# Kernel optimization log

Hardware: AMD Instinct MI355X
Metric: run time of the kernel (lower is better)

## Reference

```python
import jax, jax.numpy as jnp
import numpy as np

N, IN, D, H, L, G, FF, E = 50000, 100, 128, 8, 3, 64, 512, 800000


def setup_inputs() -> dict:
    key = jax.random.key(0)
    ks = jax.random.split(key, 12)
    s = 0.02
    x = jax.random.normal(ks[0], (N, IN), dtype=jnp.float32)
    edge_index = jax.random.randint(ks[1], (2, E), 0, N)
    batch = jnp.sort(jax.random.randint(ks[2], (N,), 0, G))
    emb_W = jax.random.normal(ks[3], (IN, D), dtype=jnp.float32) * s
    Wqk = jax.random.normal(ks[4], (L, D, 2 * D), dtype=jnp.float32) * s
    Wv = jax.random.normal(ks[5], (L, D, D), dtype=jnp.float32) * s
    Wo = jax.random.normal(ks[6], (L, D, D), dtype=jnp.float32) * s
    bo = jnp.zeros((L, D), dtype=jnp.float32)
    W1 = jax.random.normal(ks[7], (L, D, FF), dtype=jnp.float32) * s
    b1 = jnp.zeros((L, FF), dtype=jnp.float32)
    W2 = jax.random.normal(ks[8], (L, FF, D), dtype=jnp.float32) * s
    b2 = jnp.zeros((L, D), dtype=jnp.float32)
    return {"x": x, "emb_W": emb_W, "Wqk": Wqk, "Wv": Wv, "Wo": Wo, "bo": bo,
            "W1": W1, "b1": b1, "W2": W2, "b2": b2,
            "edge_index": edge_index, "batch": batch}


def reference(x, emb_W, Wqk, Wv, Wo, bo, W1, b1, W2, b2, edge_index, batch):
    n = x.shape[0]
    d = emb_W.shape[1]
    n_layers = Wqk.shape[0]
    n_heads = H
    hd = d // n_heads
    scale = hd ** (-0.5)
    src, dst = edge_index[0], edge_index[1]  # PyG: j=source, i=target

    h = x @ emb_W  # [n, d]  (dropout is identity in eval)
    for l in range(n_layers):
        qk = h @ Wqk[l]  # [n, 2d]; chunk0 -> _j (source), chunk1 -> _i (target)
        q = qk[:, :d].reshape(n, n_heads, hd)
        k = qk[:, d:].reshape(n, n_heads, hd)
        v = (h @ Wv[l]).reshape(n, n_heads, hd)
        # per-edge attention scores [E, H]
        scores = jnp.sum(k[dst] * q[src], axis=-1) * scale
        # segment softmax over edges sharing a destination node
        m = jax.ops.segment_max(scores, dst, num_segments=n)
        ex = jnp.exp(scores - m[dst])
        denom = jax.ops.segment_sum(ex, dst, num_segments=n)
        attn = ex / (denom[dst] + 1e-16)  # utils.softmax adds 1e-16
        msg = v[src] * attn[:, :, None]  # [E, H, hd]
        out = jax.ops.segment_sum(msg, dst, num_segments=n).reshape(n, d)
        out = out @ Wo[l] + bo[l]
        h = h + out  # norm1 = Identity (batch_norm=True)
        ff = jax.nn.relu(h @ W1[l] + b1[l]) @ W2[l] + b2[l]
        h = h + ff  # norm2 = Identity
    # global mean pool per graph
    n_graphs = G
    sums = jax.ops.segment_sum(h, batch, num_segments=n_graphs)
    cnt = jax.ops.segment_sum(jnp.ones((n, 1), h.dtype), batch, num_segments=n_graphs)
    return sums / jnp.maximum(cnt, 1.0)
```

## Files before the change

kernel.cpp:

```cpp
#include <hip/hip_runtime.h>
#include <math.h>

#define NN 50000
#define NPAD 50048
#define IN_DIM 100
#define DD 128
#define HH 8
#define LL 3
#define GG 64
#define FFD 512
#define EE 800000

typedef __attribute__((ext_vector_type(8))) short bf8_t;
typedef __attribute__((ext_vector_type(4))) float f4_t;

static __device__ __forceinline__ unsigned short f2bf(float f) {
    unsigned u = __builtin_bit_cast(unsigned, f);
    unsigned r = (u + 0x7FFFu + ((u >> 16) & 1u)) >> 16;
    return (unsigned short)r;
}
static __device__ __forceinline__ float bf2f(unsigned short b) {
    unsigned u = ((unsigned)b) << 16;
    return __builtin_bit_cast(float, u);
}

#define GLD16(gsrc, ldst) __builtin_amdgcn_global_load_lds( \
    (const __attribute__((address_space(1))) unsigned int*)(gsrc), \
    (__attribute__((address_space(3))) unsigned int*)(ldst), 16, 0, 0)

__global__ __launch_bounds__(256) void mfma_gemm(
    const unsigned short* __restrict__ Ac,
    const unsigned short* __restrict__ Bc,
    const float* __restrict__ bias,
    const float* __restrict__ resid,
    float* __restrict__ Cf,
    unsigned short* __restrict__ Chl,
    unsigned short* __restrict__ Cb,
    int n, int nk, int M, int do_relu)
{
    __shared__ unsigned short ldsA[128 * 64];
    __shared__ unsigned short ldsB[128 * 64];
    const int tid = threadIdx.x;
    const int lane = tid & 63;
    const int wid = tid >> 6;
    const int wr = (wid >> 1) * 64;
    const int wc = (wid & 1) * 64;
    const long brow = (long)blockIdx.x * 128;
    const long bcol = (long)blockIdx.y * 128;

    f4_t acc[4][4] = {};

    const int srow = tid >> 3;
    const int kbg = (((tid & 7) << 4) ^ ((srow & 7) << 4)) >> 1;
    const int fr = lane & 15;
    const int kq = (lane >> 4) << 4;

    for (int kc = 0; kc < nk; ++kc) {
#pragma unroll
        for (int i = 0; i < 4; ++i) {
            int row = i * 32 + srow;
            GLD16(Ac + ((brow + row) * (size_t)nk + kc) * 64 + kbg,
                  &ldsA[((size_t)i * 256 + tid) * 8]);
            GLD16(Bc + ((bcol + row) * (size_t)nk + kc) * 64 + kbg,
                  &ldsB[((size_t)i * 256 + tid) * 8]);
        }
        __syncthreads();

        bf8_t ah[4], al[4], bh[4], bl[4];
#pragma unroll
        for (int m = 0; m < 4; ++m) {
            int row = wr + m * 16 + fr;
            int sw = (row & 7) << 4;
            ah[m] = *(const bf8_t*)&ldsA[row * 64 + ((kq ^ sw) >> 1)];
            al[m] = *(const bf8_t*)&ldsA[row * 64 + (((kq + 64) ^ sw) >> 1)];
        }
#pragma unroll
        for (int nn = 0; nn < 4; ++nn) {
            int row = wc + nn * 16 + fr;
            int sw = (row & 7) << 4;
            bh[nn] = *(const bf8_t*)&ldsB[row * 64 + ((kq ^ sw) >> 1)];
            bl[nn] = *(const bf8_t*)&ldsB[row * 64 + (((kq + 64) ^ sw) >> 1)];
        }
#pragma unroll
        for (int m = 0; m < 4; ++m)
#pragma unroll
            for (int nn = 0; nn < 4; ++nn) {
                acc[m][nn] = __builtin_amdgcn_mfma_f32_16x16x32_bf16(ah[m], bh[nn], acc[m][nn], 0, 0, 0);
                acc[m][nn] = __builtin_amdgcn_mfma_f32_16x16x32_bf16(al[m], bh[nn], acc[m][nn], 0, 0, 0);
                acc[m][nn] = __builtin_amdgcn_mfma_f32_16x16x32_bf16(ah[m], bl[nn], acc[m][nn], 0, 0, 0);
            }
        __syncthreads();
    }

    const int efr = lane & 15, efq = lane >> 4;
#pragma unroll
    for (int m = 0; m < 4; ++m) {
#pragma unroll
        for (int i = 0; i < 4; ++i) {
            long row = brow + wr + m * 16 + efq * 4 + i;
            if (row >= n) continue;
#pragma unroll
            for (int nn = 0; nn < 4; ++nn) {
                int col = (int)bcol + wc + nn * 16 + efr;
                float v = acc[m][nn][i];
                if (bias) v += bias[col];
                if (do_relu) v = fmaxf(v, 0.f);
                if (resid) v += resid[row * M + col];
                if (Cf) Cf[row * M + col] = v;
                if (Cb) Cb[row * M + col] = f2bf(v);
                if (Chl) {
                    unsigned short hb = f2bf(v);
                    float lo = v - bf2f(hb);
                    size_t cb = (row * (size_t)(M >> 5) + (col >> 5)) * 64 + (col & 31);
                    Chl[cb] = hb;
                    Chl[cb + 32] = f2bf(lo);
                }
            }
        }
    }
}

#define FF_STAGE(T, BUF) do {                                                   \
    _Pragma("unroll")                                                           \
    for (int i_ = 0; i_ < 4; ++i_) {                                            \
        int row_ = i_ * 32 + srow;                                              \
        const unsigned short* srcp_;                                            \
        if ((T) < 4) {                                                          \
            srcp_ = WoT + ((size_t)row_ * 4 + (T)) * 64 + kbg;                  \
        } else {                                                                \
            const int tt_ = (T) - 4;                                            \
            const int c_ = tt_ >> 3, ph_ = (tt_ >> 2) & 1, j_ = tt_ & 3;        \
            srcp_ = (ph_ == 0)                                                  \
                ? W1T + (((size_t)c_ * 128 + row_) * 4 + j_) * 64 + kbg         \
                : W2T + ((size_t)row_ * 16 + (c_ * 4 + j_)) * 64 + kbg;         \
        }                                                                       \
        GLD16(srcp_, &ldsB[BUF][((size_t)i_ * 256 + tid) * 8]);                 \
    }                                                                           \
} while (0)

__global__ __launch_bounds__(256, 2) void ffwo_fused(
    const unsigned short* __restrict__ acp,
    const unsigned short* __restrict__ WoT,
    const unsigned short* __restrict__ W1T,
    const unsigned short* __restrict__ W2T,
    const float* __restrict__ bo,
    const float* __restrict__ b1,
    const float* __restrict__ b2,
    float* __restrict__ h,
    unsigned short* __restrict__ hcout,
    int n)
{
    __shared__ unsigned short ldsB[2][128 * 64];
    __shared__ unsigned short midb[64 * 128];
    __shared__ unsigned short Ahi[64 * 128];

    const int tid = threadIdx.x;
    const int lane = tid & 63;
    const int wid = tid >> 6;
    const int wr = (wid >> 1) * 32;
    const int wc = (wid & 1) * 64;
    const long brow = (long)blockIdx.x * 64;

    const int srow = tid >> 3;
    const int kbg = (((tid & 7) << 4) ^ ((srow & 7) << 4)) >> 1;
    const int fr = lane & 15;
    const int kq = (lane >> 4) << 4;
    const int kq4 = lane >> 4;
    const int efr = lane & 15, efq = lane >> 4;

    bf8_t ahw[2][4];
#pragma unroll
    for (int m = 0; m < 2; ++m) {
        long arow = brow + wr + m * 16 + fr;
#pragma unroll
        for (int kc = 0; kc < 4; ++kc)
            ahw[m][kc] = *(const bf8_t*)&acp[arow * 128 + kc * 32 + kq4 * 8];
    }

    FF_STAGE(0, 0);

    f4_t accW[2][4];
    f4_t acc1[2][4];
    f4_t acc2[2][4];
    f4_t hnew[2][4];
#pragma unroll
    for (int m = 0; m < 2; ++m)
#pragma unroll
        for (int nn = 0; nn < 4; ++nn) {
            accW[m][nn][0] = 0.f; accW[m][nn][1] = 0.f;
            accW[m][nn][2] = 0.f; accW[m][nn][3] = 0.f;
            acc2[m][nn][0] = 0.f; acc2[m][nn][1] = 0.f;
            acc2[m][nn][2] = 0.f; acc2[m][nn][3] = 0.f;
        }

    __syncthreads();

#pragma unroll
    for (int t = 0; t < 36; ++t) {
        const int cur = t & 1;
        if (t < 35) FF_STAGE(t + 1, cur ^ 1);

        if (t < 4) {
            bf8_t bh[4], bl[4];
#pragma unroll
            for (int nn = 0; nn < 4; ++nn) {
                int rowb = wc + nn * 16 + fr;
                int sw = (rowb & 7) << 4;
                bh[nn] = *(const bf8_t*)&ldsB[cur][rowb * 64 + ((kq ^ sw) >> 1)];
                bl[nn] = *(const bf8_t*)&ldsB[cur][rowb * 64 + (((kq + 64) ^ sw) >> 1)];
            }
#pragma unroll
            for (int m = 0; m < 2; ++m)
#pragma unroll
                for (int nn = 0; nn < 4; ++nn) {
                    accW[m][nn] = __builtin_amdgcn_mfma_f32_16x16x32_bf16(ahw[m][t], bh[nn], accW[m][nn], 0, 0, 0);
                    accW[m][nn] = __builtin_amdgcn_mfma_f32_16x16x32_bf16(ahw[m][t], bl[nn], accW[m][nn], 0, 0, 0);
                }
            if (t == 3) {
#pragma unroll
                for (int m = 0; m < 2; ++m)
#pragma unroll
                    for (int i = 0; i < 4; ++i) {
                        int lrow = wr + m * 16 + efq * 4 + i;
                        long row = brow + lrow;
#pragma unroll
                        for (int nn = 0; nn < 4; ++nn) {
                            int col = wc + nn * 16 + efr;
                            float v = accW[m][nn][i] + bo[col] + h[row * 128 + col];
                            hnew[m][nn][i] = v;
                            Ahi[(lrow << 7) + ((((col << 1) ^ ((lrow & 7) << 4))) >> 1)] = f2bf(v);
                        }
                    }
            }
        } else {
            const int tt = t - 4, c = tt >> 3, ph = (tt >> 2) & 1, j = tt & 3;
            if (ph == 0) {
                if (j == 0) {
#pragma unroll
                    for (int m = 0; m < 2; ++m)
#pragma unroll
                        for (int nn = 0; nn < 4; ++nn) {
                            acc1[m][nn][0] = 0.f; acc1[m][nn][1] = 0.f;
                            acc1[m][nn][2] = 0.f; acc1[m][nn][3] = 0.f;
                        }
                }
                bf8_t ah[2], bh[4], bl[4];
#pragma unroll
                for (int m = 0; m < 2; ++m) {
                    int lrow = wr + m * 16 + fr;
                    int kbyte = (j * 64 + kq) ^ ((lrow & 7) << 4);
                    ah[m] = *(const bf8_t*)&Ahi[(lrow << 7) + (kbyte >> 1)];
                }
#pragma unroll
                for (int nn = 0; nn < 4; ++nn) {
                    int rowb = wc + nn * 16 + fr;
                    int sw = (rowb & 7) << 4;
                    bh[nn] = *(const bf8_t*)&ldsB[cur][rowb * 64 + ((kq ^ sw) >> 1)];
                    bl[nn] = *(const bf8_t*)&ldsB[cur][rowb * 64 + (((kq + 64) ^ sw) >> 1)];
                }
#pragma unroll
                for (int m = 0; m < 2; ++m)
#pragma unroll
                    for (int nn = 0; nn < 4; ++nn) {
                        acc1[m][nn] = __builtin_amdgcn_mfma_f32_16x16x32_bf16(ah[m], bh[nn], acc1[m][nn], 0, 0, 0);
                        acc1[m][nn] = __builtin_amdgcn_mfma_f32_16x16x32_bf16(ah[m], bl[nn], acc1[m][nn], 0, 0, 0);
                    }
                if (j == 3) {
#pragma unroll
                    for (int m = 0; m < 2; ++m)
#pragma unroll
                        for (int i = 0; i < 4; ++i) {
                            int lrow = wr + m * 16 + efq * 4 + i;
#pragma unroll
                            for (int nn = 0; nn < 4; ++nn) {
                                int col = wc + nn * 16 + efr;
                                float v = fmaxf(acc1[m][nn][i] + b1[c * 128 + col], 0.f);
                                int e2 = (lrow << 7) + ((((col << 1) ^ ((lrow & 7) << 4))) >> 1);
                                midb[e2] = f2bf(v);
                            }
                        }
                }
            } else {
                bf8_t am[2], bh2[4], bl2[4];
#pragma unroll
                for (int m = 0; m < 2; ++m) {
                    int lrow = wr + m * 16 + fr;
                    int kbyte = (j * 64 + kq) ^ ((lrow & 7) << 4);
                    am[m] = *(const bf8_t*)&midb[(lrow << 7) + (kbyte >> 1)];
                }
#pragma unroll
                for (int nn = 0; nn < 4; ++nn) {
                    int rowb = wc + nn * 16 + fr;
                    int sw = (rowb & 7) << 4;
                    bh2[nn] = *(const bf8_t*)&ldsB[cur][rowb * 64 + ((kq ^ sw) >> 1)];
                    bl2[nn] = *(const bf8_t*)&ldsB[cur][rowb * 64 + (((kq + 64) ^ sw) >> 1)];
                }
#pragma unroll
                for (int m = 0; m < 2; ++m)
#pragma unroll
                    for (int nn = 0; nn < 4; ++nn) {
                        acc2[m][nn] = __builtin_amdgcn_mfma_f32_16x16x32_bf16(am[m], bh2[nn], acc2[m][nn], 0, 0, 0);
                        acc2[m][nn] = __builtin_amdgcn_mfma_f32_16x16x32_bf16(am[m], bl2[nn], acc2[m][nn], 0, 0, 0);
                    }
            }
        }
        __syncthreads();
    }

#pragma unroll
    for (int m = 0; m < 2; ++m)
#pragma unroll
        for (int i = 0; i < 4; ++i) {
            long row = brow + wr + m * 16 + efq * 4 + i;
            if (row >= n) continue;
#pragma unroll
            for (int nn = 0; nn < 4; ++nn) {
                int col = wc + nn * 16 + efr;
                float v = hnew[m][nn][i] + acc2[m][nn][i] + b2[col];
                h[row * 128 + col] = v;
                if (hcout) {
                    unsigned short hb = f2bf(v);
                    size_t cb = (row * (size_t)4 + (col >> 5)) * 64 + (col & 31);
                    hcout[cb] = hb;
                    hcout[cb + 32] = f2bf(v - bf2f(hb));
                }
            }
        }
}

__global__ void cvt_x_kernel(const float* __restrict__ x, unsigned short* __restrict__ xc)
{
    int idx = blockIdx.x * 256 + threadIdx.x;
    if (idx >= NN * 128) return;
    int node = idx >> 7, col = idx & 127;
    float v = (col < IN_DIM) ? x[(size_t)node * IN_DIM + col] : 0.f;
    unsigned short hb = f2bf(v);
    float lo = v - bf2f(hb);
    size_t b = (size_t)node * 256 + (col >> 5) * 64 + (col & 31);
    xc[b] = hb;
    xc[b + 32] = f2bf(lo);
}

struct WDesc { const float* W; unsigned short* Wt; int K, nkpad, M, base; };
struct WDescs { WDesc d[16]; int n; int total; };

__global__ void wcvt_all_kernel(WDescs ds)
{
    int idx = blockIdx.x * 256 + threadIdx.x;
    if (idx >= ds.total) return;
    int di = 0;
    while (di + 1 < ds.n && idx >= ds.d[di + 1].base) ++di;
    WDesc w = ds.d[di];
    int loc = idx - w.base;
    int m = loc % w.M;
    int kc = loc / w.M;
    size_t ob = ((size_t)m * w.nkpad + kc) * 64;
    for (int i = 0; i < 32; ++i) {
        int k = kc * 32 + i;
        float v = (k < w.K) ? w.W[(size_t)k * w.M + m] : 0.f;
        unsigned short hb = f2bf(v);
        w.Wt[ob + i] = hb;
        w.Wt[ob + 32 + i] = f2bf(v - bf2f(hb));
    }
}

__global__ void count_kernel(const int* __restrict__ dst, int* __restrict__ counts)
{
    int e = blockIdx.x * 256 + threadIdx.x;
    if (e < EE) atomicAdd(&counts[dst[e]], 1);
}

__global__ __launch_bounds__(1024) void scan1_kernel(
    const int* __restrict__ counts, int* __restrict__ offsets, int* __restrict__ bsums)
{
    __shared__ int buf[1024];
    int tid = threadIdx.x;
    int i = blockIdx.x * 1024 + tid;
    int v = (i < NN) ? counts[i] : 0;
    buf[tid] = v;
    __syncthreads();
    for (int off = 1; off < 1024; off <<= 1) {
        int t = (tid >= off) ? buf[tid - off] : 0;
        __syncthreads();
        buf[tid] += t;
        __syncthreads();
    }
    if (i < NN) offsets[i + 1] = buf[tid];
    if (tid == 1023) bsums[blockIdx.x] = buf[1023];
}

__global__ void scan2_kernel(int* __restrict__ bsums, int nb)
{
    __shared__ int buf[64];
    int tid = threadIdx.x;
    int v = (tid < nb) ? bsums[tid] : 0;
    buf[tid] = v;
    __syncthreads();
    for (int off = 1; off < 64; off <<= 1) {
        int t = (tid >= off) ? buf[tid - off] : 0;
        __syncthreads();
        buf[tid] += t;
        __syncthreads();
    }
    if (tid < nb) bsums[tid] = buf[tid] - v;
}

__global__ __launch_bounds__(1024) void scan3_kernel(
    int* __restrict__ offsets, const int* __restrict__ bsums)
{
    int i = blockIdx.x * 1024 + threadIdx.x;
    if (i < NN) offsets[i + 1] += bsums[blockIdx.x];
    if (i == 0) offsets[0] = 0;
}

__global__ void fill_kernel(const int* __restrict__ src, const int* __restrict__ dst,
                            const int* __restrict__ offsets, int* __restrict__ cursor,
                            int* __restrict__ csr_src)
{
    int e = blockIdx.x * 256 + threadIdx.x;
    if (e < EE) {
        int d = dst[e];
        int pos = atomicAdd(&cursor[d], 1);
        csr_src[offsets[d] + pos] = src[e];
    }
}

__global__ __launch_bounds__(256) void attn_kernel(
    const unsigned short* __restrict__ QKV,
    const int* __restrict__ offsets, const int* __restrict__ csr_src,
    unsigned short* __restrict__ ac)
{
    int wave = threadIdx.x >> 6;
    int lane = threadIdx.x & 63;
    int node = blockIdx.x * 4 + wave;
    if (node >= NN) return;
    int qoff = ((lane >> 3) << 4) + ((lane & 7) << 1);
    ushort2 k2 = *(const ushort2*)&QKV[(size_t)node * 384 + 128 + qoff];
    float kx = bf2f(k2.x), ky = bf2f(k2.y);
    float m = -INFINITY, s = 0.f, a0 = 0.f, a1 = 0.f;
    int e = offsets[node], end = offsets[node + 1];
    for (; e + 3 < end; e += 4) {
        int j0 = csr_src[e], j1 = csr_src[e + 1], j2 = csr_src[e + 2], j3 = csr_src[e + 3];
        ushort2 q0 = *(const ushort2*)&QKV[(size_t)j0 * 384 + qoff];
        ushort2 q1 = *(const ushort2*)&QKV[(size_t)j1 * 384 + qoff];
        ushort2 q2 = *(const ushort2*)&QKV[(size_t)j2 * 384 + qoff];
        ushort2 q3 = *(const ushort2*)&QKV[(size_t)j3 * 384 + qoff];
        ushort2 v0 = *(const ushort2*)&QKV[(size_t)j0 * 384 + 256 + qoff];
        ushort2 v1 = *(const ushort2*)&QKV[(size_t)j1 * 384 + 256 + qoff];
        ushort2 v2 = *(const ushort2*)&QKV[(size_t)j2 * 384 + 256 + qoff];
        ushort2 v3 = *(const ushort2*)&QKV[(size_t)j3 * 384 + 256 + qoff];
        float p0 = kx * bf2f(q0.x) + ky * bf2f(q0.y);
        float p1 = kx * bf2f(q1.x) + ky * bf2f(q1.y);
        float p2 = kx * bf2f(q2.x) + ky * bf2f(q2.y);
        float p3 = kx * bf2f(q3.x) + ky * bf2f(q3.y);
        p0 += __shfl_xor(p0, 1, 64); p0 += __shfl_xor(p0, 2, 64); p0 += __shfl_xor(p0, 4, 64);
        p1 += __shfl_xor(p1, 1, 64); p1 += __shfl_xor(p1, 2, 64); p1 += __shfl_xor(p1, 4, 64);
        p2 += __shfl_xor(p2, 1, 64); p2 += __shfl_xor(p2, 2, 64); p2 += __shfl_xor(p2, 4, 64);
        p3 += __shfl_xor(p3, 1, 64); p3 += __shfl_xor(p3, 2, 64); p3 += __shfl_xor(p3, 4, 64);
        float sc0 = p0 * 0.25f, sc1 = p1 * 0.25f, sc2 = p2 * 0.25f, sc3 = p3 * 0.25f;
        float mx = fmaxf(fmaxf(fmaxf(sc0, sc1), fmaxf(sc2, sc3)), m);
        float corr = __expf(m - mx);
        float w0 = __expf(sc0 - mx), w1 = __expf(sc1 - mx);
        float w2 = __expf(sc2 - mx), w3 = __expf(sc3 - mx);
        s  = s  * corr + (w0 + w1) + (w2 + w3);
        a0 = a0 * corr + w0 * bf2f(v0.x) + w1 * bf2f(v1.x) + w2 * bf2f(v2.x) + w3 * bf2f(v3.x);
        a1 = a1 * corr + w0 * bf2f(v0.y) + w1 * bf2f(v1.y) + w2 * bf2f(v2.y) + w3 * bf2f(v3.y);
        m = mx;
    }
    if (e + 1 < end) {
        int j0 = csr_src[e], j1 = csr_src[e + 1];
        ushort2 q0 = *(const ushort2*)&QKV[(size_t)j0 * 384 + qoff];
        ushort2 v0 = *(const ushort2*)&QKV[(size_t)j0 * 384 + 256 + qoff];
        ushort2 q1 = *(const ushort2*)&QKV[(size_t)j1 * 384 + qoff];
        ushort2 v1 = *(const ushort2*)&QKV[(size_t)j1 * 384 + 256 + qoff];
        float p0 = kx * bf2f(q0.x) + ky * bf2f(q0.y);
        float p1 = kx * bf2f(q1.x) + ky * bf2f(q1.y);
        p0 += __shfl_xor(p0, 1, 64); p0 += __shfl_xor(p0, 2, 64); p0 += __shfl_xor(p0, 4, 64);
        p1 += __shfl_xor(p1, 1, 64); p1 += __shfl_xor(p1, 2, 64); p1 += __shfl_xor(p1, 4, 64);
        float sc0 = p0 * 0.25f, sc1 = p1 * 0.25f;
        float mn = fmaxf(m, fmaxf(sc0, sc1));
        float corr = __expf(m - mn);
        float w0 = __expf(sc0 - mn), w1 = __expf(sc1 - mn);
        s  = s  * corr + w0 + w1;
        a0 = a0 * corr + w0 * bf2f(v0.x) + w1 * bf2f(v1.x);
        a1 = a1 * corr + w0 * bf2f(v0.y) + w1 * bf2f(v1.y);
        m = mn;
        e += 2;
    }
    if (e < end) {
        int j = csr_src[e];
        ushort2 qj = *(const ushort2*)&QKV[(size_t)j * 384 + qoff];
        ushort2 vj = *(const ushort2*)&QKV[(size_t)j * 384 + 256 + qoff];
        float p = kx * bf2f(qj.x) + ky * bf2f(qj.y);
        p += __shfl_xor(p, 1, 64); p += __shfl_xor(p, 2, 64); p += __shfl_xor(p, 4, 64);
        float score = p * 0.25f;
        float mn = fmaxf(m, score);
        float corr = __expf(m - mn);
        float w = __expf(score - mn);
        s  = s  * corr + w;
        a0 = a0 * corr + w * bf2f(vj.x);
        a1 = a1 * corr + w * bf2f(vj.y);
        m = mn;
    }
    float inv = 1.f / (s + 1e-16f);
    ushort2 o;
    o.x = f2bf(a0 * inv);
    o.y = f2bf(a1 * inv);
    *(ushort2*)&ac[(size_t)node * 128 + qoff] = o;
}

__global__ __launch_bounds__(256) void pool_kernel(
    const float* __restrict__ h, const int* __restrict__ batch,
    float* __restrict__ sums, int* __restrict__ cnts)
{
    int tid = threadIdx.x;
    int c4 = tid & 31;
    int rs = tid >> 5;
    int start = blockIdx.x * 256;
    int r0 = start + rs;
    if (r0 >= NN) return;
    int lim = min(start + 256, NN);
    float4 acc = make_float4(0.f, 0.f, 0.f, 0.f);
    int cnt = 0;
    int cur = batch[r0];
    for (int r = r0; r < lim; r += 8) {
        int g = batch[r];
        if (g != cur) {
            atomicAdd(&sums[cur * DD + c4 * 4 + 0], acc.x);
            atomicAdd(&sums[cur * DD + c4 * 4 + 1], acc.y);
            atomicAdd(&sums[cur * DD + c4 * 4 + 2], acc.z);
            atomicAdd(&sums[cur * DD + c4 * 4 + 3], acc.w);
            if (c4 == 0) atomicAdd(&cnts[cur], cnt);
            acc = make_float4(0.f, 0.f, 0.f, 0.f);
            cnt = 0; cur = g;
        }
        float4 v = *(const float4*)&h[(size_t)r * DD + c4 * 4];
        acc.x += v.x; acc.y += v.y; acc.z += v.z; acc.w += v.w;
        ++cnt;
    }
    atomicAdd(&sums[cur * DD + c4 * 4 + 0], acc.x);
    atomicAdd(&sums[cur * DD + c4 * 4 + 1], acc.y);
    atomicAdd(&sums[cur * DD + c4 * 4 + 2], acc.z);
    atomicAdd(&sums[cur * DD + c4 * 4 + 3], acc.w);
    if (c4 == 0) atomicAdd(&cnts[cur], cnt);
}

__global__ void finalize_kernel(const float* __restrict__ sums, const int* __restrict__ cnts,
                                float* __restrict__ out)
{
    int g = blockIdx.x, c = threadIdx.x;
    out[g * DD + c] = sums[g * DD + c] / fmaxf((float)cnts[g], 1.f);
}

extern "C" void kernel_launch(void* const* d_in, const int* in_sizes, int n_in,
                              void* d_out, int out_size, void* d_ws, size_t ws_size,
                              hipStream_t stream)
{
    const float* x     = (const float*)d_in[0];
    const float* emb_W = (const float*)d_in[1];
    const float* Wqk   = (const float*)d_in[2];
    const float* Wv    = (const float*)d_in[3];
    const float* Wo    = (const float*)d_in[4];
    const float* bo    = (const float*)d_in[5];
    const float* W1    = (const float*)d_in[6];
    const float* b1    = (const float*)d_in[7];
    const float* W2    = (const float*)d_in[8];
    const float* b2    = (const float*)d_in[9];
    const int* eidx    = (const int*)d_in[10];
    const int* batch   = (const int*)d_in[11];
    float* out = (float*)d_out;

    char* base = (char*)d_ws;
    size_t off = 0;
    auto alloc = [&](size_t bytes) { char* p = base + off; off = (off + bytes + 255) & ~(size_t)255; return p; };

    float*          h    = (float*)alloc((size_t)NPAD * DD * 4);
    unsigned short* hc   = (unsigned short*)alloc((size_t)NPAD * 2 * DD * 2);
    char*           regB = alloc((size_t)NPAD * 384 * 2 + (size_t)NPAD * 128 * 2 + 256);
    unsigned short* xc   = (unsigned short*)regB;
    unsigned short* QKVb = (unsigned short*)regB;
    unsigned short* acp  = (unsigned short*)(regB + (size_t)NPAD * 384 * 2);

    unsigned short* WqkvT = (unsigned short*)alloc((size_t)LL * 384 * 256 * 2);
    unsigned short* WoT   = (unsigned short*)alloc((size_t)LL * 128 * 256 * 2);
    unsigned short* W1T   = (unsigned short*)alloc((size_t)LL * 512 * 256 * 2);
    unsigned short* W2T   = (unsigned short*)alloc((size_t)LL * 128 * 1024 * 2);
    unsigned short* embT  = (unsigned short*)alloc((size_t)128 * 256 * 2);

    int* counts  = (int*)alloc((NN + 1) * 4);
    int* offsets = (int*)alloc((NN + 1) * 4);
    int* cursor  = (int*)alloc(NN * 4);
    int* bsums   = (int*)alloc(64 * 4);
    int* csr_src = (int*)alloc((size_t)EE * 4);
    float* sums  = (float*)alloc(GG * DD * 4 + GG * 4);
    int* cnts    = (int*)(sums + GG * DD);

    const int* src = eidx;
    const int* dst = eidx + EE;

    hipMemsetAsync(counts, 0, (NN + 1) * sizeof(int), stream);
    hipMemsetAsync(cursor, 0, NN * sizeof(int), stream);
    hipMemsetAsync(sums, 0, GG * DD * sizeof(float) + GG * sizeof(int), stream);

    const int NB1 = (NN + 1023) / 1024;
    count_kernel<<<dim3((EE + 255) / 256), dim3(256), 0, stream>>>(dst, counts);
    scan1_kernel<<<dim3(NB1), dim3(1024), 0, stream>>>(counts, offsets, bsums);
    scan2_kernel<<<dim3(1), dim3(64), 0, stream>>>(bsums, NB1);
    scan3_kernel<<<dim3(NB1), dim3(1024), 0, stream>>>(offsets, bsums);
    fill_kernel<<<dim3((EE + 255) / 256), dim3(256), 0, stream>>>(src, dst, offsets, cursor, csr_src);

    WDescs ds;
    int b = 0, di = 0;
    auto addw = [&](const float* W, unsigned short* Wt, int K, int nkpad, int M) {
        ds.d[di].W = W; ds.d[di].Wt = Wt; ds.d[di].K = K;
        ds.d[di].nkpad = nkpad; ds.d[di].M = M; ds.d[di].base = b;
        b += M * nkpad; ++di;
    };
    addw(emb_W, embT, IN_DIM, 4, DD);
    for (int l = 0; l < LL; ++l) {
        addw(Wqk + (size_t)l * DD * 256, WqkvT + (size_t)l * 384 * 256, DD, 4, 256);
        addw(Wv  + (size_t)l * DD * DD,  WqkvT + (size_t)l * 384 * 256 + 256 * 256, DD, 4, 128);
        addw(Wo  + (size_t)l * DD * DD,  WoT + (size_t)l * 128 * 256, DD, 4, 128);
        addw(W1  + (size_t)l * DD * FFD, W1T + (size_t)l * 512 * 256, DD, 4, 512);
        addw(W2  + (size_t)l * FFD * DD, W2T + (size_t)l * 128 * 1024, FFD, 16, 128);
    }
    ds.n = di; ds.total = b;
    wcvt_all_kernel<<<dim3((b + 255) / 256), dim3(256), 0, stream>>>(ds);

    cvt_x_kernel<<<dim3((NN * 128 + 255) / 256), dim3(256), 0, stream>>>(x, xc);

    dim3 blk(256);
    const int gx = (NN + 127) / 128;
    const int gx2 = (NN + 63) / 64;

    mfma_gemm<<<dim3(gx, 1), blk, 0, stream>>>(
        xc, embT, nullptr, nullptr, h, hc, nullptr, NN, 4, DD, 0);

    for (int l = 0; l < LL; ++l) {
        mfma_gemm<<<dim3(gx, 3), blk, 0, stream>>>(
            hc, WqkvT + (size_t)l * 384 * 256, nullptr, nullptr,
            nullptr, nullptr, QKVb, NN, 4, 384, 0);
        attn_kernel<<<dim3(NN / 4), blk, 0, stream>>>(QKVb, offsets, csr_src, acp);
        ffwo_fused<<<dim3(gx2), blk, 0, stream>>>(
            acp, WoT + (size_t)l * 128 * 256,
            W1T + (size_t)l * 512 * 256, W2T + (size_t)l * 128 * 1024,
            bo + (size_t)l * DD, b1 + (size_t)l * FFD, b2 + (size_t)l * DD, h,
            (l == LL - 1) ? nullptr : hc, NN);
    }

    pool_kernel<<<dim3((NN + 255) / 256), blk, 0, stream>>>(h, batch, sums, cnts);
    finalize_kernel<<<dim3(GG), dim3(128), 0, stream>>>(sums, cnts, out);
}
```

Baseline: 740.2 us.

## Use 512-thread 128-row tiles for QKV and fused FFN kernels

```diff
diff --git a/kernel.cpp b/kernel.cpp
--- a/kernel.cpp
+++ b/kernel.cpp
@@ -120,10 +120,96 @@
     }
 }
 
-#define FF_STAGE(T, BUF) do {                                                   \
+__global__ __launch_bounds__(512, 4) void qkv_gemm(
+    const unsigned short* __restrict__ hc,
+    const unsigned short* __restrict__ WqkvT,
+    unsigned short* __restrict__ QKVb,
+    int n)
+{
+    __shared__ unsigned short ldsA[4][128 * 64];
+    __shared__ unsigned short ldsB[128 * 64];
+    const int tid = threadIdx.x;
+    const int lane = tid & 63;
+    const int wid = tid >> 6;
+    const int wr = (wid >> 1) * 32;
+    const int wc = (wid & 1) * 64;
+    const long brow = (long)blockIdx.x * 128;
+
+    const int srow = tid >> 3;
+    const int kbg = (((tid & 7) << 4) ^ ((srow & 7) << 4)) >> 1;
+    const int fr = lane & 15;
+    const int kq = (lane >> 4) << 4;
+    const int efr = lane & 15, efq = lane >> 4;
+
+#pragma unroll
+    for (int kc = 0; kc < 4; ++kc) {
+#pragma unroll
+        for (int i = 0; i < 2; ++i) {
+            int lin = i * 512 + tid;
+            int row = lin >> 3;
+            GLD16(hc + ((brow + row) * (size_t)4 + kc) * 64 + kbg,
+                  &ldsA[kc][(size_t)lin * 8]);
+        }
+    }
+    __syncthreads();
+
+    for (int colb = 0; colb < 3; ++colb) {
+        f4_t acc[2][4] = {};
+        for (int kc = 0; kc < 4; ++kc) {
+#pragma unroll
+            for (int i = 0; i < 2; ++i) {
+                int lin = i * 512 + tid;
+                int row = lin >> 3;
+                GLD16(WqkvT + (((size_t)colb * 128 + row) * 4 + kc) * 64 + kbg,
+                      &ldsB[(size_t)lin * 8]);
+            }
+            __syncthreads();
+
+            bf8_t ah[2], al[2], bh[4], bl[4];
+#pragma unroll
+            for (int m = 0; m < 2; ++m) {
+                int row = wr + m * 16 + fr;
+                int sw = (row & 7) << 4;
+                ah[m] = *(const bf8_t*)&ldsA[kc][row * 64 + ((kq ^ sw) >> 1)];
+                al[m] = *(const bf8_t*)&ldsA[kc][row * 64 + (((kq + 64) ^ sw) >> 1)];
+            }
+#pragma unroll
+            for (int nn = 0; nn < 4; ++nn) {
+                int row = wc + nn * 16 + fr;
+                int sw = (row & 7) << 4;
+                bh[nn] = *(const bf8_t*)&ldsB[row * 64 + ((kq ^ sw) >> 1)];
+                bl[nn] = *(const bf8_t*)&ldsB[row * 64 + (((kq + 64) ^ sw) >> 1)];
+            }
+#pragma unroll
+            for (int m = 0; m < 2; ++m)
+#pragma unroll
+                for (int nn = 0; nn < 4; ++nn) {
+                    acc[m][nn] = __builtin_amdgcn_mfma_f32_16x16x32_bf16(ah[m], bh[nn], acc[m][nn], 0, 0, 0);
+                    acc[m][nn] = __builtin_amdgcn_mfma_f32_16x16x32_bf16(al[m], bh[nn], acc[m][nn], 0, 0, 0);
+                    acc[m][nn] = __builtin_amdgcn_mfma_f32_16x16x32_bf16(ah[m], bl[nn], acc[m][nn], 0, 0, 0);
+                }
+            __syncthreads();
+        }
+#pragma unroll
+        for (int m = 0; m < 2; ++m)
+#pragma unroll
+            for (int i = 0; i < 4; ++i) {
+                long row = brow + wr + m * 16 + efq * 4 + i;
+                if (row >= n) continue;
+#pragma unroll
+                for (int nn = 0; nn < 4; ++nn) {
+                    int col = colb * 128 + wc + nn * 16 + efr;
+                    QKVb[row * 384 + col] = f2bf(acc[m][nn][i]);
+                }
+            }
+    }
+}
+
+#define FF_STAGE(T) do {                                                        \
     _Pragma("unroll")                                                           \
-    for (int i_ = 0; i_ < 4; ++i_) {                                            \
-        int row_ = i_ * 32 + srow;                                              \
+    for (int i_ = 0; i_ < 2; ++i_) {                                            \
+        int lin_ = i_ * 512 + tid;                                              \
+        int row_ = lin_ >> 3;                                                   \
         const unsigned short* srcp_;                                            \
         if ((T) < 4) {                                                          \
             srcp_ = WoT + ((size_t)row_ * 4 + (T)) * 64 + kbg;                  \
@@ -134,11 +220,11 @@
                 ? W1T + (((size_t)c_ * 128 + row_) * 4 + j_) * 64 + kbg         \
                 : W2T + ((size_t)row_ * 16 + (c_ * 4 + j_)) * 64 + kbg;         \
         }                                                                       \
-        GLD16(srcp_, &ldsB[BUF][((size_t)i_ * 256 + tid) * 8]);                 \
+        GLD16(srcp_, &ldsB[(size_t)lin_ * 8]);                                  \
     }                                                                           \
 } while (0)
 
-__global__ __launch_bounds__(256, 2) void ffwo_fused(
+__global__ __launch_bounds__(512, 4) void ffwo_fused(
     const unsigned short* __restrict__ acp,
     const unsigned short* __restrict__ WoT,
     const unsigned short* __restrict__ W1T,
@@ -150,16 +236,16 @@
     unsigned short* __restrict__ hcout,
     int n)
 {
-    __shared__ unsigned short ldsB[2][128 * 64];
-    __shared__ unsigned short midb[64 * 128];
-    __shared__ unsigned short Ahi[64 * 128];
+    __shared__ unsigned short ldsB[128 * 64];
+    __shared__ unsigned short midb[128 * 128];
+    __shared__ unsigned short Ahi[128 * 128];
 
     const int tid = threadIdx.x;
     const int lane = tid & 63;
     const int wid = tid >> 6;
     const int wr = (wid >> 1) * 32;
     const int wc = (wid & 1) * 64;
-    const long brow = (long)blockIdx.x * 64;
+    const long brow = (long)blockIdx.x * 128;
 
     const int srow = tid >> 3;
     const int kbg = (((tid & 7) << 4) ^ ((srow & 7) << 4)) >> 1;
@@ -177,8 +263,6 @@
             ahw[m][kc] = *(const bf8_t*)&acp[arow * 128 + kc * 32 + kq4 * 8];
     }
 
-    FF_STAGE(0, 0);
-
     f4_t accW[2][4];
     f4_t acc1[2][4];
     f4_t acc2[2][4];
@@ -193,12 +277,10 @@
             acc2[m][nn][2] = 0.f; acc2[m][nn][3] = 0.f;
         }
 
-    __syncthreads();
-
 #pragma unroll
     for (int t = 0; t < 36; ++t) {
-        const int cur = t & 1;
-        if (t < 35) FF_STAGE(t + 1, cur ^ 1);
+        FF_STAGE(t);
+        __syncthreads();
 
         if (t < 4) {
             bf8_t bh[4], bl[4];
@@ -206,8 +288,8 @@
             for (int nn = 0; nn < 4; ++nn) {
                 int rowb = wc + nn * 16 + fr;
                 int sw = (rowb & 7) << 4;
-                bh[nn] = *(const bf8_t*)&ldsB[cur][rowb * 64 + ((kq ^ sw) >> 1)];
-                bl[nn] = *(const bf8_t*)&ldsB[cur][rowb * 64 + (((kq + 64) ^ sw) >> 1)];
+                bh[nn] = *(const bf8_t*)&ldsB[rowb * 64 + ((kq ^ sw) >> 1)];
+                bl[nn] = *(const bf8_t*)&ldsB[rowb * 64 + (((kq + 64) ^ sw) >> 1)];
             }
 #pragma unroll
             for (int m = 0; m < 2; ++m)
@@ -255,8 +337,8 @@
                 for (int nn = 0; nn < 4; ++nn) {
                     int rowb = wc + nn * 16 + fr;
                     int sw = (rowb & 7) << 4;
-                    bh[nn] = *(const bf8_t*)&ldsB[cur][rowb * 64 + ((kq ^ sw) >> 1)];
-                    bl[nn] = *(const bf8_t*)&ldsB[cur][rowb * 64 + (((kq + 64) ^ sw) >> 1)];
+                    bh[nn] = *(const bf8_t*)&ldsB[rowb * 64 + ((kq ^ sw) >> 1)];
+                    bl[nn] = *(const bf8_t*)&ldsB[rowb * 64 + (((kq + 64) ^ sw) >> 1)];
                 }
 #pragma unroll
                 for (int m = 0; m < 2; ++m)
@@ -292,8 +374,8 @@
                 for (int nn = 0; nn < 4; ++nn) {
                     int rowb = wc + nn * 16 + fr;
                     int sw = (rowb & 7) << 4;
-                    bh2[nn] = *(const bf8_t*)&ldsB[cur][rowb * 64 + ((kq ^ sw) >> 1)];
-                    bl2[nn] = *(const bf8_t*)&ldsB[cur][rowb * 64 + (((kq + 64) ^ sw) >> 1)];
+                    bh2[nn] = *(const bf8_t*)&ldsB[rowb * 64 + ((kq ^ sw) >> 1)];
+                    bl2[nn] = *(const bf8_t*)&ldsB[rowb * 64 + (((kq + 64) ^ sw) >> 1)];
                 }
 #pragma unroll
                 for (int m = 0; m < 2; ++m)
@@ -630,18 +712,17 @@
     cvt_x_kernel<<<dim3((NN * 128 + 255) / 256), dim3(256), 0, stream>>>(x, xc);
 
     dim3 blk(256);
+    dim3 blk512(512);
     const int gx = (NN + 127) / 128;
-    const int gx2 = (NN + 63) / 64;
 
     mfma_gemm<<<dim3(gx, 1), blk, 0, stream>>>(
         xc, embT, nullptr, nullptr, h, hc, nullptr, NN, 4, DD, 0);
 
     for (int l = 0; l < LL; ++l) {
-        mfma_gemm<<<dim3(gx, 3), blk, 0, stream>>>(
-            hc, WqkvT + (size_t)l * 384 * 256, nullptr, nullptr,
-            nullptr, nullptr, QKVb, NN, 4, 384, 0);
+        qkv_gemm<<<dim3(gx), blk512, 0, stream>>>(
+            hc, WqkvT + (size_t)l * 384 * 256, QKVb, NN);
         attn_kernel<<<dim3(NN / 4), blk, 0, stream>>>(QKVb, offsets, csr_src, acp);
-        ffwo_fused<<<dim3(gx2), blk, 0, stream>>>(
+        ffwo_fused<<<dim3(gx), blk512, 0, stream>>>(
             acp, WoT + (size_t)l * 128 * 256,
             W1T + (size_t)l * 512 * 256, W2T + (size_t)l * 128 * 1024,
             bo + (size_t)l * DD, b1 + (size_t)l * FFD, b2 + (size_t)l * DD, h,
```

Measured after the change: 784.5 us. 6.0% more time.
